# Kernel optimization log

Hardware: AMD Instinct MI355X
Metric: run time of the kernel (lower is better)

Reference implementation:

```python
import jax, jax.numpy as jnp
import numpy as np

TEMPERATURE = 0.07
EPS = 1e-8  # torch F.cosine_similarity eps


def setup_inputs() -> dict:
    key = jax.random.key(0)
    k1, k2 = jax.random.split(key)
    N, D = 4096, 256
    z1 = jax.random.normal(k1, (N, D), dtype=jnp.float32)
    z2 = jax.random.normal(k2, (N, D), dtype=jnp.float32)
    return {"z1": z1, "z2": z2}


def reference(z1, z2):
    N = z1.shape[0]
    z = jnp.concatenate([z1, z2], axis=0)  # (2N, D)
    # cosine similarity = normalize(z) @ normalize(z).T (with eps clamp on norms)
    norms = jnp.maximum(jnp.linalg.norm(z, axis=-1, keepdims=True), EPS)
    zn = z / norms
    sim = (zn @ zn.T) / TEMPERATURE  # (2N, 2N)
    twoN = 2 * N
    eye = jnp.eye(twoN, dtype=bool)
    sim = jnp.where(eye, -1e9, sim)
    pos = jnp.concatenate([jnp.arange(N, twoN), jnp.arange(0, N)])
    # cross entropy with integer targets, mean reduction
    logZ = jax.nn.logsumexp(sim, axis=-1)  # (2N,)
    pos_logit = jnp.take_along_axis(sim, pos[:, None], axis=1)[:, 0]
    loss = jnp.mean(logZ - pos_logit)
    return loss
```

## Files before the change

### kernel.cpp

```cpp
#include <hip/hip_runtime.h>

#define N2   8192
#define DDIM 256
#define NBLK 64
#define NTRI 2080

static constexpr float INV_T = 1.0f / 0.07f;

using bf16x8 = __attribute__((ext_vector_type(8))) __bf16;
using f32x4  = __attribute__((ext_vector_type(4))) float;
using u16x8  = __attribute__((ext_vector_type(8))) unsigned short;
using u16x4  = __attribute__((ext_vector_type(4))) unsigned short;
typedef unsigned short u16;
typedef unsigned int   u32;

__device__ __forceinline__ u16 f2bf(float f) {
    u32 u = __float_as_uint(f);
    u32 r = (u + 0x7fffu + ((u >> 16) & 1u)) >> 16;
    return (u16)r;
}

__global__ void ntx_norm(const float* __restrict__ z1, const float* __restrict__ z2,
                         u16* __restrict__ zn)
{
    const int w    = threadIdx.x >> 6;
    const int lane = threadIdx.x & 63;
    const int row  = blockIdx.x * 4 + w;

    const float* src = (row < 4096) ? (z1 + (size_t)row * DDIM)
                                    : (z2 + (size_t)(row - 4096) * DDIM);
    float4 v = *(const float4*)(src + lane * 4);
    float ss = v.x * v.x + v.y * v.y + v.z * v.z + v.w * v.w;
    #pragma unroll
    for (int m = 1; m < 64; m <<= 1) ss += __shfl_xor(ss, m, 64);

    float nrm = sqrtf(ss);
    float inv = 1.0f / fmaxf(nrm, 1e-8f);

    u16x4 o;
    o.x = f2bf(v.x * inv); o.y = f2bf(v.y * inv);
    o.z = f2bf(v.z * inv); o.w = f2bf(v.w * inv);
    *(u16x4*)(zn + (size_t)row * DDIM + lane * 4) = o;
}

__global__ __launch_bounds__(256, 3)
void ntx_gemm(const u16* __restrict__ zn, float* __restrict__ partials,
              float* __restrict__ pos)
{
    __shared__ u16 lsA[128][64];
    __shared__ u16 lsB[128][64];

    const int tid  = threadIdx.x;
    const int lane = tid & 63;
    const int w    = tid >> 6;
    const int wr   = w >> 1;
    const int wc   = w & 1;

    const int t = (int)blockIdx.x;
    int br = (int)((129.0f - sqrtf(16641.0f - 8.0f * (float)t)) * 0.5f);
    while ((br + 1) * (129 - (br + 1)) / 2 <= t) ++br;
    while (br * (129 - br) / 2 > t) --br;
    const int bc = br + (t - br * (129 - br) / 2);

    const int r8  = lane >> 3;
    const int c16 = (lane & 7) * 16;

    const int fr  = lane & 15;
    const int kl  = lane >> 4;
    const int swz = (fr & 7) << 4;

    u16x8 ra[4], rb[4];

    auto gload = [&](int kt) {
        const char* base = (const char*)zn;
        #pragma unroll
        for (int tt = 0; tt < 4; ++tt) {
            const int rl = w * 32 + tt * 8 + r8;
            ra[tt] = *(const u16x8*)(base + (size_t)(br * 128 + rl) * 512 + kt * 128 + c16);
            rb[tt] = *(const u16x8*)(base + (size_t)(bc * 128 + rl) * 512 + kt * 128 + c16);
        }
    };
    auto swrite = [&]() {
        #pragma unroll
        for (int tt = 0; tt < 4; ++tt) {
            const int rl  = w * 32 + tt * 8 + r8;
            const int off = c16 ^ ((rl & 7) << 4);
            *(u16x8*)((char*)&lsA[0][0] + rl * 128 + off) = ra[tt];
            *(u16x8*)((char*)&lsB[0][0] + rl * 128 + off) = rb[tt];
        }
    };

    f32x4 acc[4][4] = {};

    gload(0);
    swrite();
    __syncthreads();

    #pragma unroll
    for (int kt = 0; kt < 4; ++kt) {
        if (kt < 3) gload(kt + 1);
        #pragma unroll
        for (int ks = 0; ks < 2; ++ks) {
            const int kb = ks * 64 + kl * 16;
            bf16x8 af[4], bv[4];
            #pragma unroll
            for (int mf = 0; mf < 4; ++mf) {
                const int r = wr * 64 + mf * 16 + fr;
                af[mf] = *(const bf16x8*)((const char*)&lsA[0][0] + r * 128 + (kb ^ swz));
            }
            #pragma unroll
            for (int nf = 0; nf < 4; ++nf) {
                const int c = wc * 64 + nf * 16 + fr;
                bv[nf] = *(const bf16x8*)((const char*)&lsB[0][0] + c * 128 + (kb ^ swz));
            }
            #pragma unroll
            for (int mf = 0; mf < 4; ++mf)
                #pragma unroll
                for (int nf = 0; nf < 4; ++nf)
                    acc[mf][nf] = __builtin_amdgcn_mfma_f32_16x16x32_bf16(
                        af[mf], bv[nf], acc[mf][nf], 0, 0, 0);
        }
        if (kt < 3) {
            __syncthreads();
            swrite();
            __syncthreads();
        }
    }

    const bool offdiag = (br != bc);
    const bool posblk  = (bc == br + 32);
    float colsum[4] = {0.f, 0.f, 0.f, 0.f};

    #pragma unroll
    for (int mf = 0; mf < 4; ++mf) {
        float rs[4] = {0.f, 0.f, 0.f, 0.f};
        const int rowq = br * 128 + wr * 64 + mf * 16 + kl * 4;
        #pragma unroll
        for (int nf = 0; nf < 4; ++nf) {
            const int col = bc * 128 + wc * 64 + nf * 16 + fr;
            f32x4 a = acc[mf][nf];
            #pragma unroll
            for (int j = 0; j < 4; ++j) {
                float e = (rowq + j == col) ? 0.f : __expf((a[j] - 1.0f) * INV_T);
                rs[j]       += e;
                colsum[nf]  += e;
                if (posblk && (rowq + j + 4096 == col)) {
                    pos[rowq + j] = a[j];
                    pos[col]      = a[j];
                }
            }
        }
        #pragma unroll
        for (int m = 1; m < 16; m <<= 1) {
            #pragma unroll
            for (int j = 0; j < 4; ++j) rs[j] += __shfl_xor(rs[j], m, 64);
        }
        if (fr == 0) {
            float* p = partials + (size_t)rowq * 128 + bc * 2 + wc;
            p[0]   = rs[0];
            p[128] = rs[1];
            p[256] = rs[2];
            p[384] = rs[3];
        }
    }

    if (offdiag) {
        #pragma unroll
        for (int m = 16; m < 64; m <<= 1) {
            #pragma unroll
            for (int nf = 0; nf < 4; ++nf) colsum[nf] += __shfl_xor(colsum[nf], m, 64);
        }
        if (kl == 0) {
            #pragma unroll
            for (int nf = 0; nf < 4; ++nf) {
                const int col = bc * 128 + wc * 64 + nf * 16 + fr;
                partials[(size_t)col * 128 + br * 2 + wr] = colsum[nf];
            }
        }
    }
}

__global__ void ntx_loss(const float* __restrict__ partials, const float* __restrict__ pos,
                         float* __restrict__ loss)
{
    const int w    = threadIdx.x >> 6;
    const int lane = threadIdx.x & 63;
    const int row  = blockIdx.x * 4 + w;

    float S = partials[(size_t)row * 128 + lane] + partials[(size_t)row * 128 + 64 + lane];
    #pragma unroll
    for (int m = 1; m < 64; m <<= 1) S += __shfl_xor(S, m, 64);

    if (lane == 0)
        loss[row] = __logf(S) + INV_T - pos[row] * INV_T;
}

__global__ void ntx_reduce(const float* __restrict__ loss, float* __restrict__ out)
{
    __shared__ float sm[1024];
    const int t = threadIdx.x;
    float s = 0.f;
    for (int i = t; i < N2; i += 1024) s += loss[i];
    sm[t] = s;
    __syncthreads();
    for (int wdt = 512; wdt > 0; wdt >>= 1) {
        if (t < wdt) sm[t] += sm[t + wdt];
        __syncthreads();
    }
    if (t == 0) out[0] = sm[0] * (1.0f / (float)N2);
}

extern "C" void kernel_launch(void* const* d_in, const int* in_sizes, int n_in,
                              void* d_out, int out_size, void* d_ws, size_t ws_size,
                              hipStream_t stream)
{
    const float* z1 = (const float*)d_in[0];
    const float* z2 = (const float*)d_in[1];
    float* out = (float*)d_out;

    u16*   zn       = (u16*)d_ws;
    float* partials = (float*)((char*)d_ws + (size_t)N2 * 512);
    float* loss     = (float*)((char*)d_ws + 2 * (size_t)N2 * 512);
    float* pos      = loss + N2;

    ntx_norm  <<<N2 / 4, 256, 0, stream>>>(z1, z2, zn);
    ntx_gemm  <<<NTRI, 256, 0, stream>>>(zn, partials, pos);
    ntx_loss  <<<N2 / 4, 256, 0, stream>>>(partials, pos, loss);
    ntx_reduce<<<1, 1024, 0, stream>>>(loss, out);
}
```

Before: 47.78 us.

## Use 256x256 triangular tiles with direct global-to-LDS double-buffered loads

Enlarges the symmetric-GEMM tile from 128x128 to 256x256 with 512-thread blocks, cutting the triangular grid from 2080 to 528 blocks. Operands are now staged with global_load_lds into double-buffered LDS instead of going through registers and a separate shared-memory write. Row and column partial sums go to separate buffers, and the loss kernel masks partials by block index. This aims to raise operand reuse and overlap loads with MFMA work, at the cost of more LDS and registers per block, fewer blocks to balance across CUs, and a heavier epilogue per block.

```diff
diff --git a/kernel.cpp b/kernel.cpp
--- a/kernel.cpp
+++ b/kernel.cpp
@@ -2,17 +2,20 @@
 
 #define N2   8192
 #define DDIM 256
-#define NBLK 64
-#define NTRI 2080
+#define NBLK 32
+#define NTRI 528
 
 static constexpr float INV_T = 1.0f / 0.07f;
 
 using bf16x8 = __attribute__((ext_vector_type(8))) __bf16;
 using f32x4  = __attribute__((ext_vector_type(4))) float;
-using u16x8  = __attribute__((ext_vector_type(8))) unsigned short;
 using u16x4  = __attribute__((ext_vector_type(4))) unsigned short;
 typedef unsigned short u16;
 typedef unsigned int   u32;
+
+#define GL2LDS(gp, lp) __builtin_amdgcn_global_load_lds( \
+    (const __attribute__((address_space(1))) void*)(gp), \
+    (__attribute__((address_space(3))) void*)(lp), 16, 0, 0)
 
 __device__ __forceinline__ u16 f2bf(float f) {
     u32 u = __float_as_uint(f);
@@ -34,8 +37,7 @@
     #pragma unroll
     for (int m = 1; m < 64; m <<= 1) ss += __shfl_xor(ss, m, 64);
 
-    float nrm = sqrtf(ss);
-    float inv = 1.0f / fmaxf(nrm, 1e-8f);
+    float inv = 1.0f / fmaxf(sqrtf(ss), 1e-8f);
 
     u16x4 o;
     o.x = f2bf(v.x * inv); o.y = f2bf(v.y * inv);
@@ -43,110 +45,99 @@
     *(u16x4*)(zn + (size_t)row * DDIM + lane * 4) = o;
 }
 
-__global__ __launch_bounds__(256, 3)
-void ntx_gemm(const u16* __restrict__ zn, float* __restrict__ partials,
-              float* __restrict__ pos)
-{
-    __shared__ u16 lsA[128][64];
-    __shared__ u16 lsB[128][64];
+__global__ __launch_bounds__(512, 2)
+void ntx_gemm(const u16* __restrict__ zn, float* __restrict__ rowp,
+              float* __restrict__ colp, float* __restrict__ pos)
+{
+    __shared__ u16 lsA[2][16384];
+    __shared__ u16 lsB[2][16384];
 
     const int tid  = threadIdx.x;
     const int lane = tid & 63;
     const int w    = tid >> 6;
-    const int wr   = w >> 1;
-    const int wc   = w & 1;
+    const int wr   = w >> 2;
+    const int wc   = w & 3;
 
     const int t = (int)blockIdx.x;
-    int br = (int)((129.0f - sqrtf(16641.0f - 8.0f * (float)t)) * 0.5f);
-    while ((br + 1) * (129 - (br + 1)) / 2 <= t) ++br;
-    while (br * (129 - br) / 2 > t) --br;
-    const int bc = br + (t - br * (129 - br) / 2);
-
-    const int r8  = lane >> 3;
-    const int c16 = (lane & 7) * 16;
+    int br = (int)((65.0f - sqrtf(4225.0f - 8.0f * (float)t)) * 0.5f);
+    while ((br + 1) * (65 - (br + 1)) / 2 <= t) ++br;
+    while (br * (65 - br) / 2 > t) --br;
+    const int bc = br + (t - br * (65 - br) / 2);
 
     const int fr  = lane & 15;
     const int kl  = lane >> 4;
     const int swz = (fr & 7) << 4;
 
-    u16x8 ra[4], rb[4];
-
-    auto gload = [&](int kt) {
-        const char* base = (const char*)zn;
-        #pragma unroll
-        for (int tt = 0; tt < 4; ++tt) {
-            const int rl = w * 32 + tt * 8 + r8;
-            ra[tt] = *(const u16x8*)(base + (size_t)(br * 128 + rl) * 512 + kt * 128 + c16);
-            rb[tt] = *(const u16x8*)(base + (size_t)(bc * 128 + rl) * 512 + kt * 128 + c16);
+    const int srow = w * 8 + (lane >> 3);
+    const int scsw = ((lane & 7) * 16) ^ ((lane >> 3) << 4);
+
+    auto stage = [&](int buf, int kt) {
+        const char* gA = (const char*)zn + (size_t)(br * 256 + srow) * 512 + kt * 128 + scsw;
+        const char* gB = (const char*)zn + (size_t)(bc * 256 + srow) * 512 + kt * 128 + scsw;
+        u16* lA = &lsA[buf][w * 512];
+        u16* lB = &lsB[buf][w * 512];
+        #pragma unroll
+        for (int i = 0; i < 4; ++i) {
+            GL2LDS(gA + (size_t)i * 32768, lA + i * 4096);
+            GL2LDS(gB + (size_t)i * 32768, lB + i * 4096);
         }
     };
-    auto swrite = [&]() {
-        #pragma unroll
-        for (int tt = 0; tt < 4; ++tt) {
-            const int rl  = w * 32 + tt * 8 + r8;
-            const int off = c16 ^ ((rl & 7) << 4);
-            *(u16x8*)((char*)&lsA[0][0] + rl * 128 + off) = ra[tt];
-            *(u16x8*)((char*)&lsB[0][0] + rl * 128 + off) = rb[tt];
-        }
-    };
-
-    f32x4 acc[4][4] = {};
-
-    gload(0);
-    swrite();
+
+    f32x4 acc[8][4] = {};
+
+    stage(0, 0);
     __syncthreads();
 
     #pragma unroll
     for (int kt = 0; kt < 4; ++kt) {
-        if (kt < 3) gload(kt + 1);
+        const int buf = kt & 1;
+        if (kt < 3) stage(buf ^ 1, kt + 1);
         #pragma unroll
         for (int ks = 0; ks < 2; ++ks) {
             const int kb = ks * 64 + kl * 16;
-            bf16x8 af[4], bv[4];
-            #pragma unroll
-            for (int mf = 0; mf < 4; ++mf) {
-                const int r = wr * 64 + mf * 16 + fr;
-                af[mf] = *(const bf16x8*)((const char*)&lsA[0][0] + r * 128 + (kb ^ swz));
+            bf16x8 af[8], bv[4];
+            #pragma unroll
+            for (int mf = 0; mf < 8; ++mf) {
+                const int r = wr * 128 + mf * 16 + fr;
+                af[mf] = *(const bf16x8*)((const char*)&lsA[buf][0] + r * 128 + (kb ^ swz));
             }
             #pragma unroll
             for (int nf = 0; nf < 4; ++nf) {
                 const int c = wc * 64 + nf * 16 + fr;
-                bv[nf] = *(const bf16x8*)((const char*)&lsB[0][0] + c * 128 + (kb ^ swz));
-            }
-            #pragma unroll
-            for (int mf = 0; mf < 4; ++mf)
+                bv[nf] = *(const bf16x8*)((const char*)&lsB[buf][0] + c * 128 + (kb ^ swz));
+            }
+            #pragma unroll
+            for (int mf = 0; mf < 8; ++mf)
                 #pragma unroll
                 for (int nf = 0; nf < 4; ++nf)
                     acc[mf][nf] = __builtin_amdgcn_mfma_f32_16x16x32_bf16(
                         af[mf], bv[nf], acc[mf][nf], 0, 0, 0);
         }
-        if (kt < 3) {
-            __syncthreads();
-            swrite();
-            __syncthreads();
-        }
-    }
-
-    const bool offdiag = (br != bc);
-    const bool posblk  = (bc == br + 32);
+        __syncthreads();
+    }
+
+    const bool diag   = (br == bc);
+    const bool posblk = (bc == br + 16);
     float colsum[4] = {0.f, 0.f, 0.f, 0.f};
 
     #pragma unroll
-    for (int mf = 0; mf < 4; ++mf) {
+    for (int mf = 0; mf < 8; ++mf) {
         float rs[4] = {0.f, 0.f, 0.f, 0.f};
-        const int rowq = br * 128 + wr * 64 + mf * 16 + kl * 4;
+        const int rloc0 = wr * 128 + mf * 16 + kl * 4;
         #pragma unroll
         for (int nf = 0; nf < 4; ++nf) {
-            const int col = bc * 128 + wc * 64 + nf * 16 + fr;
+            const int cloc = wc * 64 + nf * 16 + fr;
             f32x4 a = acc[mf][nf];
             #pragma unroll
             for (int j = 0; j < 4; ++j) {
-                float e = (rowq + j == col) ? 0.f : __expf((a[j] - 1.0f) * INV_T);
-                rs[j]       += e;
-                colsum[nf]  += e;
-                if (posblk && (rowq + j + 4096 == col)) {
-                    pos[rowq + j] = a[j];
-                    pos[col]      = a[j];
+                const int rloc = rloc0 + j;
+                float e = (diag && rloc == cloc) ? 0.f : __expf((a[j] - 1.0f) * INV_T);
+                rs[j]      += e;
+                colsum[nf] += e;
+                if (posblk && rloc == cloc) {
+                    const int grow = br * 256 + rloc;
+                    pos[grow]        = a[j];
+                    pos[grow + 4096] = a[j];
                 }
             }
         }
@@ -156,15 +147,13 @@
             for (int j = 0; j < 4; ++j) rs[j] += __shfl_xor(rs[j], m, 64);
         }
         if (fr == 0) {
-            float* p = partials + (size_t)rowq * 128 + bc * 2 + wc;
-            p[0]   = rs[0];
-            p[128] = rs[1];
-            p[256] = rs[2];
-            p[384] = rs[3];
-        }
-    }
-
-    if (offdiag) {
+            float* p = rowp + (size_t)(br * 256 + rloc0) * 128 + bc * 4 + wc;
+            #pragma unroll
+            for (int j = 0; j < 4; ++j) p[j * 128] = rs[j];
+        }
+    }
+
+    if (!diag) {
         #pragma unroll
         for (int m = 16; m < 64; m <<= 1) {
             #pragma unroll
@@ -173,26 +162,34 @@
         if (kl == 0) {
             #pragma unroll
             for (int nf = 0; nf < 4; ++nf) {
-                const int col = bc * 128 + wc * 64 + nf * 16 + fr;
-                partials[(size_t)col * 128 + br * 2 + wr] = colsum[nf];
-            }
-        }
-    }
-}
-
-__global__ void ntx_loss(const float* __restrict__ partials, const float* __restrict__ pos,
-                         float* __restrict__ loss)
+                const int col = bc * 256 + wc * 64 + nf * 16 + fr;
+                colp[(size_t)col * 64 + br * 2 + wr] = colsum[nf];
+            }
+        }
+    }
+}
+
+__global__ void ntx_loss(const float* __restrict__ rowp, const float* __restrict__ colp,
+                         const float* __restrict__ pos, float* __restrict__ loss)
 {
     const int w    = threadIdx.x >> 6;
     const int lane = threadIdx.x & 63;
     const int row  = blockIdx.x * 4 + w;
-
-    float S = partials[(size_t)row * 128 + lane] + partials[(size_t)row * 128 + 64 + lane];
-    #pragma unroll
-    for (int m = 1; m < 64; m <<= 1) S += __shfl_xor(S, m, 64);
+    const int R    = row >> 8;
+
+    float s = 0.f;
+    float v0 = rowp[(size_t)row * 128 + lane];
+    float v1 = rowp[(size_t)row * 128 + 64 + lane];
+    float v2 = colp[(size_t)row * 64 + lane];
+    if (lane      >= 4 * R) s += v0;
+    if (lane + 64 >= 4 * R) s += v1;
+    if (lane      <  2 * R) s += v2;
+
+    #pragma unroll
+    for (int m = 1; m < 64; m <<= 1) s += __shfl_xor(s, m, 64);
 
     if (lane == 0)
-        loss[row] = __logf(S) + INV_T - pos[row] * INV_T;
+        loss[row] = __logf(s) + INV_T - pos[row] * INV_T;
 }
 
 __global__ void ntx_reduce(const float* __restrict__ loss, float* __restrict__ out)
@@ -218,13 +215,14 @@
     const float* z2 = (const float*)d_in[1];
     float* out = (float*)d_out;
 
-    u16*   zn       = (u16*)d_ws;
-    float* partials = (float*)((char*)d_ws + (size_t)N2 * 512);
-    float* loss     = (float*)((char*)d_ws + 2 * (size_t)N2 * 512);
-    float* pos      = loss + N2;
+    u16*   zn   = (u16*)d_ws;
+    float* rowp = (float*)((char*)d_ws + (4u << 20));
+    float* colp = (float*)((char*)d_ws + (8u << 20));
+    float* loss = (float*)((char*)d_ws + (10u << 20));
+    float* pos  = loss + N2;
 
     ntx_norm  <<<N2 / 4, 256, 0, stream>>>(z1, z2, zn);
-    ntx_gemm  <<<NTRI, 256, 0, stream>>>(zn, partials, pos);
-    ntx_loss  <<<N2 / 4, 256, 0, stream>>>(partials, pos, loss);
+    ntx_gemm  <<<NTRI, 512, 0, stream>>>(zn, rowp, colp, pos);
+    ntx_loss  <<<N2 / 4, 256, 0, stream>>>(rowp, colp, pos, loss);
     ntx_reduce<<<1, 1024, 0, stream>>>(loss, out);
 }
```

Measured after the change: 57.70 us. 1.21x slower.
